# Kernel tuning notes

Measured on AMD Instinct MI355X. Metric: run time of the kernel, lower is better.

## Reference

```python
import jax, jax.numpy as jnp
import numpy as np

EMBED_DIM = 1024
NUM_HEADS = 32
MULT = 2                      # edit_channel_multiply_factor
HPM = NUM_HEADS // MULT       # heads_per_multiply = 16
HEAD_DIM = EMBED_DIM * MULT // NUM_HEADS  # 64


def setup_inputs() -> dict:
    key = jax.random.key(0)
    ks = jax.random.split(key, 8)
    B, Q, S, D = 8, 4096, 128, EMBED_DIM
    return {
        "encoder_hidden_states": jax.random.normal(ks[0], (B, Q, D), dtype=jnp.float32),
        "hidden_states": jax.random.normal(ks[1], (B, S, D), dtype=jnp.float32),
        # Conv1D weights are [nx, nf] (input-major, like GPT-2), std=0.02; biases zero
        "q_w": jax.random.normal(ks[2], (MULT, D, D), dtype=jnp.float32) * 0.02,
        "q_b": jnp.zeros((MULT, D), dtype=jnp.float32),
        "c_attn_w": jax.random.normal(ks[3], (MULT, D, 2 * D), dtype=jnp.float32) * 0.02,
        "c_attn_b": jnp.zeros((MULT, 2 * D), dtype=jnp.float32),
        "c_proj_w": jax.random.normal(ks[4], (MULT, D, D), dtype=jnp.float32) * 0.02,
        "c_proj_b": jnp.zeros((MULT, D), dtype=jnp.float32),
    }


def _forward(encoder_hidden_states, hidden_states, q_w, q_b,
             c_attn_w, c_attn_b, c_proj_w, c_proj_b):
    B, Q, D = encoder_hidden_states.shape
    # last-token hidden state supplies K/V (kv_len == 1)
    h_last = hidden_states[:, -1, :]                                  # [B, D]

    # all M projections batched via einsum over the multiply dim 'm'
    q = jnp.einsum("bqe,mef->mbqf", encoder_hidden_states, q_w) \
        + q_b[:, None, None, :]                                       # [M, B, Q, D]
    kv = jnp.einsum("be,mef->mbf", h_last, c_attn_w) \
        + c_attn_b[:, None, :]                                        # [M, B, 2D]
    k, v = kv[..., :D], kv[..., D:]                                   # [M, B, D]

    # split heads: D = HPM * HEAD_DIM
    q = q.reshape(MULT, B, Q, HPM, HEAD_DIM)                          # [M,B,Q,H,d]
    k = k.reshape(MULT, B, HPM, HEAD_DIM)                             # [M,B,H,d]
    v = v.reshape(MULT, B, HPM, HEAD_DIM)

    # GPT2 eager attention with a single key: scores [M,B,H,Q] (kv=1)
    scores = jnp.einsum("mbqhd,mbhd->mbhq", q, k) / jnp.sqrt(
        jnp.asarray(HEAD_DIM, dtype=q.dtype))
    # softmax over the kv axis (size 1) -> identically 1, kept for fidelity
    w = jax.nn.softmax(scores[..., None], axis=-1)                    # [M,B,H,Q,1]
    attn = w * v[:, :, :, None, :]                                    # [M,B,H,Q,d]

    # merge heads -> [M, B, Q, D], then output projection
    attn = attn.transpose(0, 1, 3, 2, 4).reshape(MULT, B, Q, D)
    out_m = jnp.einsum("mbqd,mde->mbqe", attn, c_proj_w) \
        + c_proj_b[:, None, None, :]                                  # [M,B,Q,D]

    # faithful accumulation: outputs[0][0] += attn_output[0] for i > 0
    # (only batch element 0 receives contributions from multiplies > 0)
    out = out_m[0]
    out = out.at[0].add(jnp.sum(out_m[1:, 0], axis=0))
    return out


def reference(encoder_hidden_states, hidden_states, q_w, q_b,
              c_attn_w, c_attn_b, c_proj_w, c_proj_b):
    return _forward(encoder_hidden_states, hidden_states, q_w, q_b,
                    c_attn_w, c_attn_b, c_proj_w, c_proj_b)
```

## Files before the change

### kernel.cpp

```cpp
#include <hip/hip_runtime.h>

#define DIM    1024
#define BATCH  8
#define QLEN   4096
#define SEQ    128

typedef float vfloat4 __attribute__((ext_vector_type(4)));

__global__ void __launch_bounds__(256) kernelA(const float* __restrict__ hidden,
                                               const float* __restrict__ c_attn_w,
                                               float* __restrict__ vp) {
    __shared__ float h_s[BATCH][64];
    __shared__ vfloat4 vred[16][16][9];

    const int tid = threadIdx.x;
    const int es = blockIdx.x & 15;
    const int c  = (blockIdx.x >> 4) & 15;
    const int m  = blockIdx.x >> 8;

    if (tid < 128) {
        int b = tid >> 4, e4 = tid & 15;
        const vfloat4* src = reinterpret_cast<const vfloat4*>(
            hidden + (size_t)b * (SEQ * DIM) + (size_t)(SEQ - 1) * DIM + es * 64);
        reinterpret_cast<vfloat4*>(h_s[b])[e4] = src[e4];
    }
    __syncthreads();

    const int d4 = tid & 15;
    const int eg = tid >> 4;
    const float* wbase = c_attn_w + (size_t)m * DIM * (2 * DIM) + DIM + c * 64 + d4 * 4;

    vfloat4 acc[BATCH];
#pragma unroll
    for (int b = 0; b < BATCH; ++b) acc[b] = (vfloat4){0.f, 0.f, 0.f, 0.f};

#pragma unroll
    for (int k = 0; k < 4; ++k) {
        int el = eg * 4 + k;
        int e  = es * 64 + el;
        vfloat4 w4 = *reinterpret_cast<const vfloat4*>(wbase + (size_t)e * (2 * DIM));
#pragma unroll
        for (int b = 0; b < BATCH; ++b) acc[b] += h_s[b][el] * w4;
    }
#pragma unroll
    for (int b = 0; b < BATCH; ++b) vred[eg][d4][b] = acc[b];
    __syncthreads();

    if (tid < 128) {
        int b = tid >> 4, dq = tid & 15;
        vfloat4 s = vred[0][dq][b];
#pragma unroll
        for (int g = 1; g < 16; ++g) s += vred[g][dq][b];
        reinterpret_cast<vfloat4*>(vp)[es * 4096 + (m * BATCH + b) * 256 + c * 16 + dq] = s;
    }
}

__global__ void __launch_bounds__(256) kernelB(const float* __restrict__ vp,
                                               const float* __restrict__ c_attn_b,
                                               const float* __restrict__ c_proj_w,
                                               const float* __restrict__ c_proj_b,
                                               float* __restrict__ y) {
    __shared__ float v_s[DIM];
    __shared__ vfloat4 red[32][9];

    const int tid = threadIdx.x;
    const int ce = blockIdx.x & 31;
    const int b  = (blockIdx.x >> 5) & 7;
    const int m  = blockIdx.x >> 8;

    {
        vfloat4 s = reinterpret_cast<const vfloat4*>(
            c_attn_b + (size_t)m * 2 * DIM + DIM)[tid];
        const vfloat4* vp4 = reinterpret_cast<const vfloat4*>(vp);
#pragma unroll
        for (int es = 0; es < 16; ++es) {
            s += vp4[es * 4096 + (m * BATCH + b) * 256 + tid];
        }
        reinterpret_cast<vfloat4*>(v_s)[tid] = s;
    }
    __syncthreads();

    const int e4 = tid & 7;
    const int dg = tid >> 3;
    const float* wp = c_proj_w + (size_t)m * DIM * DIM + ce * 32 + e4 * 4;

    vfloat4 acc = {0.f, 0.f, 0.f, 0.f};
#pragma unroll 8
    for (int j = 0; j < 32; ++j) {
        int d = dg + 32 * j;
        vfloat4 w4 = *reinterpret_cast<const vfloat4*>(wp + (size_t)d * DIM);
        acc += v_s[d] * w4;
    }
    red[dg][e4] = acc;
    __syncthreads();
#pragma unroll
    for (int s = 16; s >= 1; s >>= 1) {
        if (dg < s) red[dg][e4] += red[dg + s][e4];
        __syncthreads();
    }
    if (tid < 8) {
        vfloat4 bias = reinterpret_cast<const vfloat4*>(c_proj_b)[m * 256 + ce * 8 + tid];
        reinterpret_cast<vfloat4*>(y)[(m * BATCH + b) * 256 + ce * 8 + tid] =
            red[0][tid] + bias;
    }
}

__global__ void __launch_bounds__(256) bcast_kernel(const float* __restrict__ y,
                                                    float* __restrict__ out) {
    int b = blockIdx.x >> 8;
    int q0 = (blockIdx.x & 255) * 16;
    int t = threadIdx.x;

    const vfloat4* y4 = reinterpret_cast<const vfloat4*>(y);
    vfloat4 val = y4[b * 256 + t];
    if (b == 0) {
        val += y4[BATCH * 256 + t];
    }

    vfloat4* o = reinterpret_cast<vfloat4*>(out) + ((size_t)b * QLEN + q0) * 256 + t;
#pragma unroll
    for (int q = 0; q < 16; ++q) {
        __builtin_nontemporal_store(val, o + (size_t)q * 256);
    }
}

extern "C" void kernel_launch(void* const* d_in, const int* in_sizes, int n_in,
                              void* d_out, int out_size, void* d_ws, size_t ws_size,
                              hipStream_t stream) {
    const float* hidden   = (const float*)d_in[1];
    const float* c_attn_w = (const float*)d_in[4];
    const float* c_attn_b = (const float*)d_in[5];
    const float* c_proj_w = (const float*)d_in[6];
    const float* c_proj_b = (const float*)d_in[7];
    float* out = (float*)d_out;

    float* vp = (float*)d_ws;
    float* y  = vp + 16 * 16384;

    kernelA<<<512, 256, 0, stream>>>(hidden, c_attn_w, vp);
    kernelB<<<512, 256, 0, stream>>>(vp, c_attn_b, c_proj_w, c_proj_b, y);
    bcast_kernel<<<2048, 256, 0, stream>>>(y, out);
}
```

Baseline: 41.32 us.

## Fuse output-projection GEMV with broadcast and skip unused multiply-1 batches

Merges the output-projection GEMV and the broadcast write into a single kernel, so the intermediate y buffer and one kernel launch go away. The multiply-1 branch is computed only for batch 0, the only batch that uses it, and the bias add moves into the kernel. The shared-memory tree reduction becomes a serial sum done by 8 threads. In exchange, the 128 MB broadcast is now issued by only 256 blocks. Each block writes 128-byte row segments at a 4 KB stride, which may lower store throughput compared with the earlier 2048-block broadcast that wrote full rows.

```diff
diff --git a/kernel.cpp b/kernel.cpp
--- a/kernel.cpp
+++ b/kernel.cpp
@@ -55,71 +55,71 @@
     }
 }
 
-__global__ void __launch_bounds__(256) kernelB(const float* __restrict__ vp,
-                                               const float* __restrict__ c_attn_b,
-                                               const float* __restrict__ c_proj_w,
-                                               const float* __restrict__ c_proj_b,
-                                               float* __restrict__ y) {
-    __shared__ float v_s[DIM];
+__global__ void __launch_bounds__(256) gemv_bcast(const float* __restrict__ vp,
+                                                  const float* __restrict__ c_attn_b,
+                                                  const float* __restrict__ c_proj_w,
+                                                  const float* __restrict__ c_proj_b,
+                                                  float* __restrict__ out) {
+    __shared__ float v_s[2][DIM];
     __shared__ vfloat4 red[32][9];
+    __shared__ vfloat4 y_row[8];
 
-    const int tid = threadIdx.x;
     const int ce = blockIdx.x & 31;
-    const int b  = (blockIdx.x >> 5) & 7;
-    const int m  = blockIdx.x >> 8;
+    const int b  = blockIdx.x >> 5;
+    const int t  = threadIdx.x;
 
     {
-        vfloat4 s = reinterpret_cast<const vfloat4*>(
-            c_attn_b + (size_t)m * 2 * DIM + DIM)[tid];
         const vfloat4* vp4 = reinterpret_cast<const vfloat4*>(vp);
+        vfloat4 s = reinterpret_cast<const vfloat4*>(c_attn_b + DIM)[t];
 #pragma unroll
-        for (int es = 0; es < 16; ++es) {
-            s += vp4[es * 4096 + (m * BATCH + b) * 256 + tid];
+        for (int es = 0; es < 16; ++es) s += vp4[es * 4096 + b * 256 + t];
+        reinterpret_cast<vfloat4*>(v_s[0])[t] = s;
+        if (b == 0) {
+            vfloat4 s1 = reinterpret_cast<const vfloat4*>(c_attn_b + 3 * DIM)[t];
+#pragma unroll
+            for (int es = 0; es < 16; ++es) s1 += vp4[es * 4096 + BATCH * 256 + t];
+            reinterpret_cast<vfloat4*>(v_s[1])[t] = s1;
         }
-        reinterpret_cast<vfloat4*>(v_s)[tid] = s;
     }
     __syncthreads();
 
-    const int e4 = tid & 7;
-    const int dg = tid >> 3;
-    const float* wp = c_proj_w + (size_t)m * DIM * DIM + ce * 32 + e4 * 4;
-
+    const int e4 = t & 7;
+    const int dg = t >> 3;
+    const float* wp0 = c_proj_w + ce * 32 + e4 * 4;
     vfloat4 acc = {0.f, 0.f, 0.f, 0.f};
 #pragma unroll 8
     for (int j = 0; j < 32; ++j) {
         int d = dg + 32 * j;
-        vfloat4 w4 = *reinterpret_cast<const vfloat4*>(wp + (size_t)d * DIM);
-        acc += v_s[d] * w4;
+        acc += v_s[0][d] * *reinterpret_cast<const vfloat4*>(wp0 + (size_t)d * DIM);
+    }
+    if (b == 0) {
+        const float* wp1 = c_proj_w + (size_t)DIM * DIM + ce * 32 + e4 * 4;
+#pragma unroll 8
+        for (int j = 0; j < 32; ++j) {
+            int d = dg + 32 * j;
+            acc += v_s[1][d] * *reinterpret_cast<const vfloat4*>(wp1 + (size_t)d * DIM);
+        }
     }
     red[dg][e4] = acc;
     __syncthreads();
+
+    if (t < 8) {
+        vfloat4 s = red[0][t];
 #pragma unroll
-    for (int s = 16; s >= 1; s >>= 1) {
-        if (dg < s) red[dg][e4] += red[dg + s][e4];
-        __syncthreads();
+        for (int g = 1; g < 32; ++g) s += red[g][t];
+        s += reinterpret_cast<const vfloat4*>(c_proj_b)[ce * 8 + t];
+        if (b == 0) s += reinterpret_cast<const vfloat4*>(c_proj_b)[256 + ce * 8 + t];
+        y_row[t] = s;
     }
-    if (tid < 8) {
-        vfloat4 bias = reinterpret_cast<const vfloat4*>(c_proj_b)[m * 256 + ce * 8 + tid];
-        reinterpret_cast<vfloat4*>(y)[(m * BATCH + b) * 256 + ce * 8 + tid] =
-            red[0][tid] + bias;
-    }
-}
+    __syncthreads();
 
-__global__ void __launch_bounds__(256) bcast_kernel(const float* __restrict__ y,
-                                                    float* __restrict__ out) {
-    int b = blockIdx.x >> 8;
-    int q0 = (blockIdx.x & 255) * 16;
-    int t = threadIdx.x;
-
-    const vfloat4* y4 = reinterpret_cast<const vfloat4*>(y);
-    vfloat4 val = y4[b * 256 + t];
-    if (b == 0) {
-        val += y4[BATCH * 256 + t];
-    }
-
-    vfloat4* o = reinterpret_cast<vfloat4*>(out) + ((size_t)b * QLEN + q0) * 256 + t;
-#pragma unroll
-    for (int q = 0; q < 16; ++q) {
+    vfloat4 val = y_row[e4];
+    const int qs = t >> 3;
+    vfloat4* o = reinterpret_cast<vfloat4*>(out)
+               + (size_t)b * QLEN * 256 + ce * 8 + e4;
+#pragma unroll 8
+    for (int it = 0; it < 128; ++it) {
+        int q = it * 32 + qs;
         __builtin_nontemporal_store(val, o + (size_t)q * 256);
     }
 }
@@ -135,9 +135,7 @@
     float* out = (float*)d_out;
 
     float* vp = (float*)d_ws;
-    float* y  = vp + 16 * 16384;
 
     kernelA<<<512, 256, 0, stream>>>(hidden, c_attn_w, vp);
-    kernelB<<<512, 256, 0, stream>>>(vp, c_attn_b, c_proj_w, c_proj_b, y);
-    bcast_kernel<<<2048, 256, 0, stream>>>(y, out);
+    gemv_bcast<<<256, 256, 0, stream>>>(vp, c_attn_b, c_proj_w, c_proj_b, out);
 }
```

Result: faster. 39.32 us (-4.9%).
